# Kernel optimization log

Measured on AMD Instinct MI355X. Metric: run time of the kernel, lower is better.

Reference implementation:

```python
import jax, jax.numpy as jnp
import numpy as np

B, T, HD = 128, 256, 512
N_REAL, N_CAT, N_CLASSES, EMB = 32, 4, 100, 8
COMBINED = N_REAL + N_CAT * EMB  # 64
NEG_SLOPE = 0.1


def setup_inputs() -> dict:
    key = jax.random.key(0)
    ks = jax.random.split(key, 20)
    s = lambda *d: 1.0 / np.sqrt(d[0])
    real = jax.random.normal(ks[0], (B, T, N_REAL), dtype=jnp.float32)
    cats = jax.random.randint(ks[1], (B, T, N_CAT), 0, N_CLASSES).astype(jnp.float32)
    x0 = jnp.concatenate([real, cats], axis=-1)
    u = lambda k, shp, fan: jax.random.uniform(k, shp, jnp.float32, -1.0/np.sqrt(fan), 1.0/np.sqrt(fan))
    return {
        'x0': x0,
        'emb': jax.random.normal(ks[2], (N_CAT, N_CLASSES, EMB), dtype=jnp.float32),
        'W1': u(ks[3], (COMBINED, HD), COMBINED), 'b1': u(ks[4], (HD,), COMBINED),
        'W2': u(ks[5], (HD, HD), HD), 'b2': u(ks[6], (HD,), HD),
        'Wi_f': u(ks[7], (HD, 4 * HD), HD), 'bi_f': u(ks[8], (4 * HD,), HD),
        'Wh_f': u(ks[9], (HD, 4 * HD), HD), 'bh_f': u(ks[10], (4 * HD,), HD),
        'Wi_r': u(ks[11], (HD, 4 * HD), HD), 'bi_r': u(ks[12], (4 * HD,), HD),
        'Wh_r': u(ks[13], (HD, 4 * HD), HD), 'bh_r': u(ks[14], (4 * HD,), HD),
        'W3': u(ks[15], (2 * HD, 1), 2 * HD), 'b3': u(ks[16], (1,), 2 * HD),
    }


def leaky(x):
    return jnp.where(x >= 0, x, NEG_SLOPE * x)


def lstm(x, Wi, bi, Wh, bh):
    # x: [B, T, H] -> hidden states [B, T, H]
    b, t, h = x.shape
    xg = jnp.einsum('bti,ig->btg', x, Wi) + bi + bh  # precompute input contribution
    def step(carry, xg_t):
        hk, ck = carry
        g = xg_t + hk @ Wh  # [B, 4H]
        f, i, a, o = jnp.split(g, 4, axis=-1)
        ck = jax.nn.sigmoid(f) * ck + jax.nn.sigmoid(i) * jnp.tanh(a)
        hk = jax.nn.sigmoid(o) * jnp.tanh(ck)
        return (hk, ck), hk
    init = (jnp.zeros((b, h), x.dtype), jnp.zeros((b, h), x.dtype))
    _, hs = jax.lax.scan(step, init, jnp.swapaxes(xg, 0, 1))
    return jnp.swapaxes(hs, 0, 1)


def reference(x0, emb, W1, b1, W2, b2, Wi_f, bi_f, Wh_f, bh_f, Wi_r, bi_r, Wh_r, bh_r, W3, b3):
    real_part = x0[..., :N_REAL]
    idx = x0[..., N_REAL:N_REAL + N_CAT].astype(jnp.int32)  # [B, T, N_CAT]
    emb_out = emb[jnp.arange(N_CAT), idx]                    # [B, T, N_CAT, EMB]
    emb_out = emb_out.reshape(x0.shape[0], x0.shape[1], -1)
    combined = jnp.concatenate([real_part, emb_out], axis=-1)
    x1 = leaky(combined @ W1 + b1)
    x2 = leaky(x1 @ W2 + b2)
    h_f = lstm(x2, Wi_f, bi_f, Wh_f, bh_f)
    h_r = lstm(jnp.flip(x2, axis=1), Wi_r, bi_r, Wh_r, bh_r)
    x3 = jnp.concatenate([h_f, h_r], axis=-1)
    return x3 @ W3 + b3  # [B, T, 1]
```

## Files before the change

kernel.cpp:

```cpp
#include <hip/hip_runtime.h>
#include <cstddef>

namespace {

constexpr int B  = 128;
constexpr int T  = 256;
constexpr int HD = 512;
constexpr int G  = 2048;
constexpr int TC = 32;
constexpr int XIN = 36;
constexpr int NCHUNK = T / TC;

typedef __attribute__((ext_vector_type(8))) short short8;
typedef __attribute__((ext_vector_type(4))) short short4v;
typedef __attribute__((ext_vector_type(4))) float f32x4;

union U16B { uint4 u; short8 s; };

__device__ __forceinline__ float sigmf(float x) { return 1.0f / (1.0f + expf(-x)); }
__device__ __forceinline__ float leakyf(float x) { return x >= 0.0f ? x : 0.1f * x; }

__device__ __forceinline__ unsigned short f2bf(float v) {
  union { float f; unsigned u; } x; x.f = v;
  unsigned r = x.u + 0x7fffu + ((x.u >> 16) & 1u);
  return (unsigned short)(r >> 16);
}
__device__ __forceinline__ float bf2f(unsigned short b) {
  union { unsigned u; float f; } x; x.u = ((unsigned)b) << 16; return x.f;
}

__global__ void k_prep(const float* __restrict__ src, unsigned short* __restrict__ dh,
                       unsigned short* __restrict__ dl, int K, int N) {
  __shared__ float tile[32][33];
  const int n0 = blockIdx.x * 32, k0 = blockIdx.y * 32;
  for (int i = threadIdx.y; i < 32; i += 8)
    tile[i][threadIdx.x] = src[(size_t)(k0 + i) * N + n0 + threadIdx.x];
  __syncthreads();
  for (int i = threadIdx.y; i < 32; i += 8) {
    const float v = tile[threadIdx.x][i];
    const unsigned short h = f2bf(v);
    const size_t o = (size_t)(n0 + i) * K + k0 + threadIdx.x;
    dh[o] = h;
    dl[o] = f2bf(v - bf2f(h));
  }
}

__global__ void k_prep_pack(const float* __restrict__ Whf, const float* __restrict__ Whr,
                            unsigned short* __restrict__ wpkh, unsigned short* __restrict__ wpkl) {
  const int f = blockIdx.x * 256 + threadIdx.x;
  const int l  = f & 63;
  const int ks = (f >> 6) & 15;
  const int ct = (f >> 10) & 7;
  const int ut = (f >> 13) & 15;
  const int dir = f >> 17;
  const float* src = dir ? Whr : Whf;
  const int L = ct * 16 + (l & 15);
  const int gcol = (L >> 5) * HD + ut * 32 + (L & 31);
  const int k0 = ks * 32 + (l >> 4) * 8;
  short8 hv, lv;
  #pragma unroll
  for (int j = 0; j < 8; ++j) {
    const float v = src[(size_t)(k0 + j) * G + gcol];
    const unsigned short h = f2bf(v);
    hv[j] = (short)h;
    lv[j] = (short)f2bf(v - bf2f(h));
  }
  *(short8*)&wpkh[(size_t)f * 8] = hv;
  *(short8*)&wpkl[(size_t)f * 8] = lv;
}

__global__ void k_bias(const float* __restrict__ bif, const float* __restrict__ bhf,
                       const float* __restrict__ bir, const float* __restrict__ bhr,
                       float* __restrict__ biasI) {
  const int i = blockIdx.x * 256 + threadIdx.x;
  const int d = i >> 11, n = i & 2047;
  biasI[i] = (d ? bir[n] : bif[n]) + (d ? bhr[n] : bhf[n]);
}

__global__ void k_embed_gemm1(const float* __restrict__ x0, const float* __restrict__ emb,
                              const float* __restrict__ W1, const float* __restrict__ b1,
                              unsigned short* __restrict__ x1h, unsigned short* __restrict__ x1l) {
  __shared__ float As[64][65];
  __shared__ float Bs[64][68];
  const int tid = threadIdx.x;
  const int m0 = blockIdx.x * 64, n0 = blockIdx.y * 64;

  for (int i = tid; i < 64 * 64; i += 256) {
    const int m = i >> 6, k = i & 63;
    const size_t row = (size_t)(m0 + m);
    float v;
    if (k < 32) {
      v = x0[row * XIN + k];
    } else {
      const int c = (k - 32) >> 3, e = (k - 32) & 7;
      const int idx = (int)x0[row * XIN + 32 + c];
      v = emb[(size_t)(c * 100 + idx) * 8 + e];
    }
    As[m][k] = v;
  }
  for (int j = 0; j < 4; ++j) {
    const int q = tid + 256 * j;
    const int kk = q >> 4, nq = q & 15;
    *(float4*)&Bs[kk][nq * 4] = *(const float4*)&W1[(size_t)kk * HD + n0 + nq * 4];
  }
  __syncthreads();

  const int ty = tid >> 4, tx = tid & 15;
  float acc[4][4] = {};
  #pragma unroll 8
  for (int k = 0; k < 64; ++k) {
    const float a0 = As[ty * 4 + 0][k], a1 = As[ty * 4 + 1][k];
    const float a2 = As[ty * 4 + 2][k], a3 = As[ty * 4 + 3][k];
    const float4 bv = *(const float4*)&Bs[k][tx * 4];
    acc[0][0] += a0 * bv.x; acc[0][1] += a0 * bv.y; acc[0][2] += a0 * bv.z; acc[0][3] += a0 * bv.w;
    acc[1][0] += a1 * bv.x; acc[1][1] += a1 * bv.y; acc[1][2] += a1 * bv.z; acc[1][3] += a1 * bv.w;
    acc[2][0] += a2 * bv.x; acc[2][1] += a2 * bv.y; acc[2][2] += a2 * bv.z; acc[2][3] += a2 * bv.w;
    acc[3][0] += a3 * bv.x; acc[3][1] += a3 * bv.y; acc[3][2] += a3 * bv.z; acc[3][3] += a3 * bv.w;
  }
  const float4 b4 = *(const float4*)&b1[n0 + tx * 4];
  for (int i = 0; i < 4; ++i) {
    float o[4];
    o[0] = leakyf(acc[i][0] + b4.x);
    o[1] = leakyf(acc[i][1] + b4.y);
    o[2] = leakyf(acc[i][2] + b4.z);
    o[3] = leakyf(acc[i][3] + b4.w);
    short4v hv, lv;
    #pragma unroll
    for (int p = 0; p < 4; ++p) {
      const unsigned short hb = f2bf(o[p]);
      hv[p] = (short)hb;
      lv[p] = (short)f2bf(o[p] - bf2f(hb));
    }
    const size_t off = (size_t)(m0 + ty * 4 + i) * HD + n0 + tx * 4;
    *(short4v*)&x1h[off] = hv;
    *(short4v*)&x1l[off] = lv;
  }
}

template <int MODE>
__global__ __launch_bounds__(512) void k_mm(
    const unsigned short* __restrict__ Ah, const unsigned short* __restrict__ Al,
    const unsigned short* __restrict__ Bh, const unsigned short* __restrict__ Bl,
    const float* __restrict__ bias,
    unsigned short* __restrict__ oh, unsigned short* __restrict__ ol,
    float* __restrict__ of, int c0) {
  __shared__ unsigned short As_h[128 * 40], As_l[128 * 40];
  __shared__ unsigned short Bs_h[128 * 40], Bs_l[128 * 40];
  const int tid = threadIdx.x;
  const int m0 = blockIdx.x * 128, n0 = blockIdx.y * 128;
  const int dir = MODE ? (m0 >> 12) : 0;
  const unsigned short* Bhd = Bh + (size_t)dir * G * HD;
  const unsigned short* Bld = Bl + (size_t)dir * G * HD;

  const int si = tid >> 2, sseg = tid & 3;
  int arow;
  if (MODE) {
    const int r = m0 + si;
    const int tc = (r >> 7) & 31, bb = r & 127;
    const int tg = dir ? (T - 1 - (c0 + tc)) : (c0 + tc);
    arow = bb * T + tg;
  } else {
    arow = m0 + si;
  }
  const int brow = n0 + si;

  const int lane = tid & 63;
  const int c16 = lane & 15, q = lane >> 4;
  const int w = tid >> 6;
  const int mg = w & 3, ng = w >> 2;

  f32x4 acc[2][4] = {};

  for (int k0 = 0; k0 < HD; k0 += 32) {
    __syncthreads();
    *(short8*)&As_h[si * 40 + sseg * 8] = *(const short8*)&Ah[(size_t)arow * HD + k0 + sseg * 8];
    *(short8*)&As_l[si * 40 + sseg * 8] = *(const short8*)&Al[(size_t)arow * HD + k0 + sseg * 8];
    *(short8*)&Bs_h[si * 40 + sseg * 8] = *(const short8*)&Bhd[(size_t)brow * HD + k0 + sseg * 8];
    *(short8*)&Bs_l[si * 40 + sseg * 8] = *(const short8*)&Bld[(size_t)brow * HD + k0 + sseg * 8];
    __syncthreads();

    short8 ah[2], al[2], bh[4], bl[4];
    #pragma unroll
    for (int a = 0; a < 2; ++a) {
      const int rr = (2 * mg + a) * 16 + c16;
      ah[a] = *(const short8*)&As_h[rr * 40 + q * 8];
      al[a] = *(const short8*)&As_l[rr * 40 + q * 8];
    }
    #pragma unroll
    for (int j = 0; j < 4; ++j) {
      const int rr = (4 * ng + j) * 16 + c16;
      bh[j] = *(const short8*)&Bs_h[rr * 40 + q * 8];
      bl[j] = *(const short8*)&Bs_l[rr * 40 + q * 8];
    }
    #pragma unroll
    for (int a = 0; a < 2; ++a)
      #pragma unroll
      for (int j = 0; j < 4; ++j) {
        acc[a][j] = __builtin_amdgcn_mfma_f32_16x16x32_bf16(ah[a], bh[j], acc[a][j], 0, 0, 0);
        acc[a][j] = __builtin_amdgcn_mfma_f32_16x16x32_bf16(ah[a], bl[j], acc[a][j], 0, 0, 0);
        acc[a][j] = __builtin_amdgcn_mfma_f32_16x16x32_bf16(al[a], bh[j], acc[a][j], 0, 0, 0);
      }
  }

  #pragma unroll
  for (int a = 0; a < 2; ++a) {
    #pragma unroll
    for (int j = 0; j < 4; ++j) {
      const int nn = n0 + (4 * ng + j) * 16 + c16;
      const float bv = MODE ? bias[dir * G + nn] : bias[nn];
      #pragma unroll
      for (int r = 0; r < 4; ++r) {
        const int mm = m0 + (2 * mg + a) * 16 + 4 * q + r;
        float v = acc[a][j][r] + bv;
        if (MODE) {
          of[(size_t)mm * G + nn] = v;
        } else {
          v = leakyf(v);
          const unsigned short hb = f2bf(v);
          oh[(size_t)mm * HD + nn] = hb;
          ol[(size_t)mm * HD + nn] = f2bf(v - bf2f(hb));
        }
      }
    }
  }
}

__global__ __launch_bounds__(512, 2) void k_scan(
    const float* __restrict__ xg, const unsigned short* __restrict__ wpkh,
    const unsigned short* __restrict__ wpkl, unsigned int* __restrict__ hpk,
    float* __restrict__ cbuf, float* __restrict__ part,
    const float* __restrict__ W3, int* __restrict__ flags, int c0) {
  __shared__ unsigned int hst[16 * 516];
  __shared__ float gl[128 * 17];
  __shared__ float ysum[16 * 33];

  const int tid = threadIdx.x;
  const int bid = blockIdx.x;
  const int dir = bid >> 7;
  const int ut  = (bid >> 3) & 15;
  const int bt  = bid & 7;
  const int u0 = ut * 32, b0 = bt * 16;
  const int w = tid >> 6, lane = tid & 63;
  const int r16 = lane & 15, q = lane >> 4;

  const unsigned short* wp = wpkh + ((size_t)(((dir * 16 + ut) * 8 + w) * 16) << 9) + lane * 8;
  const unsigned short* wq = wpkl + ((size_t)(((dir * 16 + ut) * 8 + w) * 16) << 9) + lane * 8;
#define LDW(K) const short8 wh##K = *(const short8*)(wp + (K) * 512); \
               const short8 wl##K = *(const short8*)(wq + (K) * 512);
  LDW(0) LDW(1) LDW(2) LDW(3) LDW(4) LDW(5) LDW(6) LDW(7)
  LDW(8) LDW(9) LDW(10) LDW(11) LDW(12) LDW(13) LDW(14) LDW(15)
#undef LDW

  const int b_l = tid >> 5, u2 = tid & 31;
  const int bg = b0 + b_l, jg = u0 + u2;
  const size_t ci = ((size_t)dir * B + bg) * HD + jg;
  float creg = (c0 == 0) ? 0.0f : cbuf[ci];
  const float w3v = W3[dir * HD + jg];
  const int fl_base = dir * 8 + bt;
  const int hb = r16 * 516 + q * 8;

#define KSTEP(K) { \
    const uint4 aa = *(const uint4*)&hst[hb + (K) * 32]; \
    const uint4 bb = *(const uint4*)&hst[hb + (K) * 32 + 4]; \
    U16B hiu, lou; \
    hiu.u.x = __builtin_amdgcn_perm(aa.y, aa.x, 0x07060302u); \
    hiu.u.y = __builtin_amdgcn_perm(aa.w, aa.z, 0x07060302u); \
    hiu.u.z = __builtin_amdgcn_perm(bb.y, bb.x, 0x07060302u); \
    hiu.u.w = __builtin_amdgcn_perm(bb.w, bb.z, 0x07060302u); \
    lou.u.x = __builtin_amdgcn_perm(aa.y, aa.x, 0x05040100u); \
    lou.u.y = __builtin_amdgcn_perm(aa.w, aa.z, 0x05040100u); \
    lou.u.z = __builtin_amdgcn_perm(bb.y, bb.x, 0x05040100u); \
    lou.u.w = __builtin_amdgcn_perm(bb.w, bb.z, 0x05040100u); \
    acc = __builtin_amdgcn_mfma_f32_16x16x32_bf16(wh##K, hiu.s, acc, 0, 0, 0); \
    acc = __builtin_amdgcn_mfma_f32_16x16x32_bf16(wh##K, lou.s, acc, 0, 0, 0); \
    acc = __builtin_amdgcn_mfma_f32_16x16x32_bf16(wl##K, hiu.s, acc, 0, 0, 0); }

  for (int tc = 0; tc < TC; ++tc) {
    const int t = c0 + tc;

    const float* xr = xg + (((size_t)dir * TC + tc) * B + bg) * G;
    const float xgf = xr[jg];
    const float xgi = xr[HD + jg];
    const float xga = xr[2 * HD + jg];
    const float xgo = xr[3 * HD + jg];

    f32x4 acc = {0.0f, 0.0f, 0.0f, 0.0f};
    if (t > 0) {
      if (tc > 0) {
        if (tid == 0) {
          while (__hip_atomic_load(&flags[(t - 1) * 16 + fl_base], __ATOMIC_RELAXED,
                                   __HIP_MEMORY_SCOPE_AGENT) < 16)
            __builtin_amdgcn_s_sleep(1);
        }
        __syncthreads();
      }
      {
        const unsigned int* hsrc = hpk + ((size_t)((t & 1) * 2 + dir) * B + b0) * HD;
        unsigned int hv[16];
        #pragma unroll
        for (int i = 0; i < 16; ++i)
          hv[i] = __hip_atomic_load(&hsrc[i * HD + tid], __ATOMIC_RELAXED,
                                    __HIP_MEMORY_SCOPE_AGENT);
        #pragma unroll
        for (int i = 0; i < 16; ++i)
          hst[i * 516 + tid] = hv[i];
      }
      __syncthreads();
      KSTEP(0) KSTEP(1) KSTEP(2) KSTEP(3) KSTEP(4) KSTEP(5) KSTEP(6) KSTEP(7)
      KSTEP(8) KSTEP(9) KSTEP(10) KSTEP(11) KSTEP(12) KSTEP(13) KSTEP(14) KSTEP(15)
      __syncthreads();
    }

    gl[(w * 16 + q * 4 + 0) * 17 + r16] = acc[0];
    gl[(w * 16 + q * 4 + 1) * 17 + r16] = acc[1];
    gl[(w * 16 + q * 4 + 2) * 17 + r16] = acc[2];
    gl[(w * 16 + q * 4 + 3) * 17 + r16] = acc[3];
    __syncthreads();

    {
      const float gf = gl[(u2) * 17 + b_l]      + xgf;
      const float gi = gl[(32 + u2) * 17 + b_l] + xgi;
      const float ga = gl[(64 + u2) * 17 + b_l] + xga;
      const float go = gl[(96 + u2) * 17 + b_l] + xgo;
      const float cn = sigmf(gf) * creg + sigmf(gi) * tanhf(ga);
      const float hn = sigmf(go) * tanhf(cn);
      creg = cn;
      const unsigned short hh = f2bf(hn);
      const unsigned int hp = ((unsigned)hh << 16) | (unsigned)f2bf(hn - bf2f(hh));
      __hip_atomic_store(&hpk[((size_t)(((t + 1) & 1) * 2 + dir) * B + bg) * HD + jg], hp,
                         __ATOMIC_RELAXED, __HIP_MEMORY_SCOPE_AGENT);
      ysum[b_l * 33 + u2] = hn * w3v;
    }
    __syncthreads();

    if (tid == 0)
      __hip_atomic_fetch_add(&flags[t * 16 + fl_base], 1, __ATOMIC_RELAXED,
                             __HIP_MEMORY_SCOPE_AGENT);
    if (tid < 16) {
      float s = 0.0f;
      #pragma unroll
      for (int i = 0; i < 32; ++i) s += ysum[tid * 33 + i];
      part[((size_t)t * 32 + dir * 16 + ut) * B + b0 + tid] = s;
    }
  }
#undef KSTEP

  cbuf[ci] = creg;
}

__global__ void k_out(const float* __restrict__ part, const float* __restrict__ b3,
                      float* __restrict__ out) {
  const int o = blockIdx.x * 256 + threadIdx.x;
  const int b = o & 127, t = o >> 7;
  float s = b3[0];
  #pragma unroll
  for (int g = 0; g < 32; ++g) s += part[((size_t)t * 32 + g) * B + b];
  out[(size_t)b * T + t] = s;
}

}

extern "C" void kernel_launch(void* const* d_in, const int* in_sizes, int n_in,
                              void* d_out, int out_size, void* d_ws, size_t ws_size,
                              hipStream_t stream) {
  const float* x0   = (const float*)d_in[0];
  const float* emb  = (const float*)d_in[1];
  const float* W1   = (const float*)d_in[2];
  const float* b1   = (const float*)d_in[3];
  const float* W2   = (const float*)d_in[4];
  const float* b2   = (const float*)d_in[5];
  const float* Wi_f = (const float*)d_in[6];
  const float* bi_f = (const float*)d_in[7];
  const float* Wh_f = (const float*)d_in[8];
  const float* bh_f = (const float*)d_in[9];
  const float* Wi_r = (const float*)d_in[10];
  const float* bi_r = (const float*)d_in[11];
  const float* Wh_r = (const float*)d_in[12];
  const float* bh_r = (const float*)d_in[13];
  const float* W3   = (const float*)d_in[14];
  const float* b3   = (const float*)d_in[15];
  float* out = (float*)d_out;

  char* wsb = (char*)d_ws;
  unsigned short* x1h  = (unsigned short*)(wsb + 0);
  unsigned short* x1l  = (unsigned short*)(wsb + 33554432);
  float*          xgf  = (float*)(wsb + 0);
  unsigned short* x2h  = (unsigned short*)(wsb + 67108864);
  unsigned short* x2l  = (unsigned short*)(wsb + 100663296);
  unsigned short* wih  = (unsigned short*)(wsb + 134217728);
  unsigned short* wil  = (unsigned short*)(wsb + 138412032);
  unsigned short* w2h  = (unsigned short*)(wsb + 142606336);
  unsigned short* w2l  = (unsigned short*)(wsb + 143130624);
  unsigned short* wpkh = (unsigned short*)(wsb + 143654912);
  unsigned short* wpkl = (unsigned short*)(wsb + 147849216);
  unsigned int*   hpk  = (unsigned int*)(wsb + 152043520);
  float*          cbuf = (float*)(wsb + 153092096);
  float*          part = (float*)(wsb + 153616384);
  float*          bia  = (float*)(wsb + 157810688);
  int*            flg  = (int*)(wsb + 157827072);

  k_prep_pack<<<dim3(1024), 256, 0, stream>>>(Wh_f, Wh_r, wpkh, wpkl);
  k_prep<<<dim3(G / 32, HD / 32), dim3(32, 8), 0, stream>>>(Wi_f, wih, wil, HD, G);
  k_prep<<<dim3(G / 32, HD / 32), dim3(32, 8), 0, stream>>>(Wi_r, wih + (size_t)G * HD, wil + (size_t)G * HD, HD, G);
  k_prep<<<dim3(HD / 32, HD / 32), dim3(32, 8), 0, stream>>>(W2, w2h, w2l, HD, HD);
  k_bias<<<dim3(16), 256, 0, stream>>>(bi_f, bh_f, bi_r, bh_r, bia);

  hipMemsetAsync(flg, 0, T * 16 * sizeof(int), stream);

  k_embed_gemm1<<<dim3(B * T / 64, HD / 64), 256, 0, stream>>>(x0, emb, W1, b1, x1h, x1l);

  k_mm<0><<<dim3(B * T / 128, HD / 128), 512, 0, stream>>>(
      x1h, x1l, w2h, w2l, b2, x2h, x2l, nullptr, 0);

  void* args[9];
  int c0 = 0;
  args[0] = (void*)&xgf;  args[1] = (void*)&wpkh; args[2] = (void*)&wpkl;
  args[3] = (void*)&hpk;  args[4] = (void*)&cbuf; args[5] = (void*)&part;
  args[6] = (void*)&W3;   args[7] = (void*)&flg;  args[8] = (void*)&c0;

  for (int c = 0; c < NCHUNK; ++c) {
    c0 = c * TC;
    k_mm<1><<<dim3(2 * TC * B / 128, G / 128), 512, 0, stream>>>(
        x2h, x2l, wih, wil, bia, nullptr, nullptr, xgf, c0);
    hipLaunchCooperativeKernel((void*)k_scan, dim3(256), dim3(512), args, 0, stream);
  }

  k_out<<<dim3(B * T / 256), 256, 0, stream>>>(part, b3, out);
}
```

Measured before the change: 1.813 ms.

## Overlap next-chunk input-gate GEMM with LSTM scan using extra warps

The scan kernel grows to 1024 threads. The second half of each block computes the next chunk's input-gate GEMM tile into a double-buffered xg buffer while the first half runs the recurrent step, so the separate k_mm<1> launch per chunk is dropped. The chunk size is halved to fit the GEMM work into the per-timestep stages, and recurrent weights are now reloaded from memory on each K step instead of held in registers. Trade-offs are more syncthreads shared by both halves, more LDS use, and extra weight load traffic on the critical serial path.

```diff
diff --git a/kernel.cpp b/kernel.cpp
--- a/kernel.cpp
+++ b/kernel.cpp
@@ -7,7 +7,7 @@
 constexpr int T  = 256;
 constexpr int HD = 512;
 constexpr int G  = 2048;
-constexpr int TC = 32;
+constexpr int TC = 16;
 constexpr int XIN = 36;
 constexpr int NCHUNK = T / TC;
 
@@ -148,7 +148,7 @@
   __shared__ unsigned short Bs_h[128 * 40], Bs_l[128 * 40];
   const int tid = threadIdx.x;
   const int m0 = blockIdx.x * 128, n0 = blockIdx.y * 128;
-  const int dir = MODE ? (m0 >> 12) : 0;
+  const int dir = MODE ? (m0 / (TC * B)) : 0;
   const unsigned short* Bhd = Bh + (size_t)dir * G * HD;
   const unsigned short* Bld = Bl + (size_t)dir * G * HD;
 
@@ -156,7 +156,7 @@
   int arow;
   if (MODE) {
     const int r = m0 + si;
-    const int tc = (r >> 7) & 31, bb = r & 127;
+    const int tc = (r >> 7) & (TC - 1), bb = r & (B - 1);
     const int tg = dir ? (T - 1 - (c0 + tc)) : (c0 + tc);
     arow = bb * T + tg;
   } else {
@@ -225,41 +225,110 @@
   }
 }
 
-__global__ __launch_bounds__(512, 2) void k_scan(
-    const float* __restrict__ xg, const unsigned short* __restrict__ wpkh,
-    const unsigned short* __restrict__ wpkl, unsigned int* __restrict__ hpk,
-    float* __restrict__ cbuf, float* __restrict__ part,
-    const float* __restrict__ W3, int* __restrict__ flags, int c0) {
+__global__ __launch_bounds__(1024, 4) void k_scan2(
+    const float* __restrict__ xg, float* __restrict__ xgn,
+    const unsigned short* __restrict__ wpkh, const unsigned short* __restrict__ wpkl,
+    unsigned int* __restrict__ hpk, float* __restrict__ cbuf,
+    float* __restrict__ part, const float* __restrict__ W3,
+    int* __restrict__ flags, int c0,
+    const unsigned short* __restrict__ x2h, const unsigned short* __restrict__ x2l,
+    const unsigned short* __restrict__ wih, const unsigned short* __restrict__ wil,
+    const float* __restrict__ bia, int dog) {
   __shared__ unsigned int hst[16 * 516];
   __shared__ float gl[128 * 17];
   __shared__ float ysum[16 * 33];
-
-  const int tid = threadIdx.x;
-  const int bid = blockIdx.x;
+  __shared__ unsigned short gAh[128 * 40], gAl[128 * 40];
+  __shared__ unsigned short gBh[128 * 40], gBl[128 * 40];
+
+  const int tid  = threadIdx.x;
+  const int half = tid >> 9;
+  const int stid = tid & 511;
+  const int bid  = blockIdx.x;
+
   const int dir = bid >> 7;
   const int ut  = (bid >> 3) & 15;
   const int bt  = bid & 7;
   const int u0 = ut * 32, b0 = bt * 16;
-  const int w = tid >> 6, lane = tid & 63;
+  const int w = stid >> 6, lane = stid & 63;
   const int r16 = lane & 15, q = lane >> 4;
-
   const unsigned short* wp = wpkh + ((size_t)(((dir * 16 + ut) * 8 + w) * 16) << 9) + lane * 8;
   const unsigned short* wq = wpkl + ((size_t)(((dir * 16 + ut) * 8 + w) * 16) << 9) + lane * 8;
-#define LDW(K) const short8 wh##K = *(const short8*)(wp + (K) * 512); \
-               const short8 wl##K = *(const short8*)(wq + (K) * 512);
-  LDW(0) LDW(1) LDW(2) LDW(3) LDW(4) LDW(5) LDW(6) LDW(7)
-  LDW(8) LDW(9) LDW(10) LDW(11) LDW(12) LDW(13) LDW(14) LDW(15)
-#undef LDW
-
-  const int b_l = tid >> 5, u2 = tid & 31;
+
+  const int b_l = stid >> 5, u2 = stid & 31;
   const int bg = b0 + b_l, jg = u0 + u2;
   const size_t ci = ((size_t)dir * B + bg) * HD + jg;
-  float creg = (c0 == 0) ? 0.0f : cbuf[ci];
+  float creg = 0.0f;
+  if (half == 0 && c0 > 0) creg = cbuf[ci];
   const float w3v = W3[dir * HD + jg];
   const int fl_base = dir * 8 + bt;
   const int hb = r16 * 516 + q * 8;
 
+  const int gsi = stid >> 2, gseg = stid & 3;
+  const int gw = stid >> 6, glane = stid & 63;
+  const int gc16 = glane & 15, gq = glane >> 4;
+  const int gmg = gw & 3, gng = gw >> 2;
+  const int c0n = c0 + TC;
+  f32x4 gacc[2][4] = {};
+
+#define GEMM_STAGE(g) { \
+    const int tt = bid * 2 + ((g) >> 4); const int ls = (g) & 15; \
+    const int m0g = (tt & 31) * 128, n0g = (tt >> 5) * 128; \
+    const int dirg = m0g >> 11; \
+    const int rr0 = m0g + gsi; \
+    const int tcc = (rr0 >> 7) & (TC - 1), bb2 = rr0 & (B - 1); \
+    const int tg = dirg ? (T - 1 - (c0n + tcc)) : (c0n + tcc); \
+    const int arow = bb2 * T + tg; \
+    const int brow = n0g + gsi; \
+    const int k0g = ls * 32; \
+    const unsigned short* Bh2 = wih + (size_t)dirg * G * HD; \
+    const unsigned short* Bl2 = wil + (size_t)dirg * G * HD; \
+    *(short8*)&gAh[gsi * 40 + gseg * 8] = *(const short8*)&x2h[(size_t)arow * HD + k0g + gseg * 8]; \
+    *(short8*)&gAl[gsi * 40 + gseg * 8] = *(const short8*)&x2l[(size_t)arow * HD + k0g + gseg * 8]; \
+    *(short8*)&gBh[gsi * 40 + gseg * 8] = *(const short8*)&Bh2[(size_t)brow * HD + k0g + gseg * 8]; \
+    *(short8*)&gBl[gsi * 40 + gseg * 8] = *(const short8*)&Bl2[(size_t)brow * HD + k0g + gseg * 8]; }
+
+#define GEMM_MFMA(g) { \
+    const int ls = (g) & 15; \
+    if (ls == 0) { \
+      _Pragma("unroll") for (int a = 0; a < 2; ++a) \
+        _Pragma("unroll") for (int j = 0; j < 4; ++j) \
+          gacc[a][j] = (f32x4){0.f, 0.f, 0.f, 0.f}; \
+    } \
+    short8 ah[2], al[2], bh4[4], bl4[4]; \
+    _Pragma("unroll") for (int a = 0; a < 2; ++a) { \
+      const int rr = (2 * gmg + a) * 16 + gc16; \
+      ah[a] = *(const short8*)&gAh[rr * 40 + gq * 8]; \
+      al[a] = *(const short8*)&gAl[rr * 40 + gq * 8]; \
+    } \
+    _Pragma("unroll") for (int j = 0; j < 4; ++j) { \
+      const int rr = (4 * gng + j) * 16 + gc16; \
+      bh4[j] = *(const short8*)&gBh[rr * 40 + gq * 8]; \
+      bl4[j] = *(const short8*)&gBl[rr * 40 + gq * 8]; \
+    } \
+    _Pragma("unroll") for (int a = 0; a < 2; ++a) \
+      _Pragma("unroll") for (int j = 0; j < 4; ++j) { \
+        gacc[a][j] = __builtin_amdgcn_mfma_f32_16x16x32_bf16(ah[a], bh4[j], gacc[a][j], 0, 0, 0); \
+        gacc[a][j] = __builtin_amdgcn_mfma_f32_16x16x32_bf16(ah[a], bl4[j], gacc[a][j], 0, 0, 0); \
+        gacc[a][j] = __builtin_amdgcn_mfma_f32_16x16x32_bf16(al[a], bh4[j], gacc[a][j], 0, 0, 0); \
+      } \
+    if (ls == 15) { \
+      const int tt = bid * 2 + ((g) >> 4); \
+      const int m0g = (tt & 31) * 128, n0g = (tt >> 5) * 128; \
+      const int dirg = m0g >> 11; \
+      _Pragma("unroll") for (int a = 0; a < 2; ++a) \
+        _Pragma("unroll") for (int j = 0; j < 4; ++j) { \
+          const int nn = n0g + (4 * gng + j) * 16 + gc16; \
+          const float bv = bia[dirg * G + nn]; \
+          _Pragma("unroll") for (int r = 0; r < 4; ++r) { \
+            const int mm = m0g + (2 * gmg + a) * 16 + 4 * gq + r; \
+            xgn[(size_t)mm * G + nn] = gacc[a][j][r] + bv; \
+          } \
+        } \
+    } }
+
 #define KSTEP(K) { \
+    const short8 whv = *(const short8*)(wp + (K) * 512); \
+    const short8 wlv = *(const short8*)(wq + (K) * 512); \
     const uint4 aa = *(const uint4*)&hst[hb + (K) * 32]; \
     const uint4 bb = *(const uint4*)&hst[hb + (K) * 32 + 4]; \
     U16B hiu, lou; \
@@ -271,53 +340,69 @@
     lou.u.y = __builtin_amdgcn_perm(aa.w, aa.z, 0x05040100u); \
     lou.u.z = __builtin_amdgcn_perm(bb.y, bb.x, 0x05040100u); \
     lou.u.w = __builtin_amdgcn_perm(bb.w, bb.z, 0x05040100u); \
-    acc = __builtin_amdgcn_mfma_f32_16x16x32_bf16(wh##K, hiu.s, acc, 0, 0, 0); \
-    acc = __builtin_amdgcn_mfma_f32_16x16x32_bf16(wh##K, lou.s, acc, 0, 0, 0); \
-    acc = __builtin_amdgcn_mfma_f32_16x16x32_bf16(wl##K, hiu.s, acc, 0, 0, 0); }
+    acc = __builtin_amdgcn_mfma_f32_16x16x32_bf16(whv, hiu.s, acc, 0, 0, 0); \
+    acc = __builtin_amdgcn_mfma_f32_16x16x32_bf16(whv, lou.s, acc, 0, 0, 0); \
+    acc = __builtin_amdgcn_mfma_f32_16x16x32_bf16(wlv, hiu.s, acc, 0, 0, 0); }
 
   for (int tc = 0; tc < TC; ++tc) {
     const int t = c0 + tc;
-
-    const float* xr = xg + (((size_t)dir * TC + tc) * B + bg) * G;
-    const float xgf = xr[jg];
-    const float xgi = xr[HD + jg];
-    const float xga = xr[2 * HD + jg];
-    const float xgo = xr[3 * HD + jg];
-
+    float xgf = 0.f, xgi = 0.f, xga = 0.f, xgo = 0.f;
     f32x4 acc = {0.0f, 0.0f, 0.0f, 0.0f};
-    if (t > 0) {
-      if (tc > 0) {
-        if (tid == 0) {
-          while (__hip_atomic_load(&flags[(t - 1) * 16 + fl_base], __ATOMIC_RELAXED,
-                                   __HIP_MEMORY_SCOPE_AGENT) < 16)
-            __builtin_amdgcn_s_sleep(1);
-        }
-        __syncthreads();
+
+    if (half == 0) {
+      const float* xr = xg + (((size_t)dir * TC + tc) * B + bg) * G;
+      xgf = xr[jg];
+      xgi = xr[HD + jg];
+      xga = xr[2 * HD + jg];
+      xgo = xr[3 * HD + jg];
+      if (tc > 0 && stid == 0) {
+        while (__hip_atomic_load(&flags[(t - 1) * 16 + fl_base], __ATOMIC_RELAXED,
+                                 __HIP_MEMORY_SCOPE_AGENT) < 16)
+          __builtin_amdgcn_s_sleep(1);
       }
-      {
+    } else if (dog) {
+      GEMM_STAGE(2 * tc)
+    }
+    __syncthreads();
+
+    if (half == 0) {
+      if (t > 0) {
         const unsigned int* hsrc = hpk + ((size_t)((t & 1) * 2 + dir) * B + b0) * HD;
         unsigned int hv[16];
         #pragma unroll
         for (int i = 0; i < 16; ++i)
-          hv[i] = __hip_atomic_load(&hsrc[i * HD + tid], __ATOMIC_RELAXED,
+          hv[i] = __hip_atomic_load(&hsrc[i * HD + stid], __ATOMIC_RELAXED,
                                     __HIP_MEMORY_SCOPE_AGENT);
         #pragma unroll
         for (int i = 0; i < 16; ++i)
-          hst[i * 516 + tid] = hv[i];
+          hst[i * 516 + stid] = hv[i];
       }
-      __syncthreads();
-      KSTEP(0) KSTEP(1) KSTEP(2) KSTEP(3) KSTEP(4) KSTEP(5) KSTEP(6) KSTEP(7)
-      KSTEP(8) KSTEP(9) KSTEP(10) KSTEP(11) KSTEP(12) KSTEP(13) KSTEP(14) KSTEP(15)
-      __syncthreads();
-    }
-
-    gl[(w * 16 + q * 4 + 0) * 17 + r16] = acc[0];
-    gl[(w * 16 + q * 4 + 1) * 17 + r16] = acc[1];
-    gl[(w * 16 + q * 4 + 2) * 17 + r16] = acc[2];
-    gl[(w * 16 + q * 4 + 3) * 17 + r16] = acc[3];
-    __syncthreads();
-
-    {
+    } else if (dog) {
+      GEMM_MFMA(2 * tc)
+    }
+    __syncthreads();
+
+    if (half == 0) {
+      if (t > 0) {
+        KSTEP(0) KSTEP(1) KSTEP(2) KSTEP(3) KSTEP(4) KSTEP(5) KSTEP(6) KSTEP(7)
+        KSTEP(8) KSTEP(9) KSTEP(10) KSTEP(11) KSTEP(12) KSTEP(13) KSTEP(14) KSTEP(15)
+      }
+    } else if (dog) {
+      GEMM_STAGE(2 * tc + 1)
+    }
+    __syncthreads();
+
+    if (half == 0) {
+      gl[(w * 16 + q * 4 + 0) * 17 + r16] = acc[0];
+      gl[(w * 16 + q * 4 + 1) * 17 + r16] = acc[1];
+      gl[(w * 16 + q * 4 + 2) * 17 + r16] = acc[2];
+      gl[(w * 16 + q * 4 + 3) * 17 + r16] = acc[3];
+    } else if (dog) {
+      GEMM_MFMA(2 * tc + 1)
+    }
+    __syncthreads();
+
+    if (half == 0) {
       const float gf = gl[(u2) * 17 + b_l]      + xgf;
       const float gi = gl[(32 + u2) * 17 + b_l] + xgi;
       const float ga = gl[(64 + u2) * 17 + b_l] + xga;
@@ -333,19 +418,23 @@
     }
     __syncthreads();
 
-    if (tid == 0)
-      __hip_atomic_fetch_add(&flags[t * 16 + fl_base], 1, __ATOMIC_RELAXED,
-                             __HIP_MEMORY_SCOPE_AGENT);
-    if (tid < 16) {
-      float s = 0.0f;
-      #pragma unroll
-      for (int i = 0; i < 32; ++i) s += ysum[tid * 33 + i];
-      part[((size_t)t * 32 + dir * 16 + ut) * B + b0 + tid] = s;
+    if (half == 0) {
+      if (stid == 0)
+        __hip_atomic_fetch_add(&flags[t * 16 + fl_base], 1, __ATOMIC_RELAXED,
+                               __HIP_MEMORY_SCOPE_AGENT);
+      if (stid < 16) {
+        float s = 0.0f;
+        #pragma unroll
+        for (int i = 0; i < 32; ++i) s += ysum[stid * 33 + i];
+        part[((size_t)t * 32 + dir * 16 + ut) * B + b0 + stid] = s;
+      }
     }
   }
 #undef KSTEP
-
-  cbuf[ci] = creg;
+#undef GEMM_MFMA
+#undef GEMM_STAGE
+
+  if (half == 0) cbuf[ci] = creg;
 }
 
 __global__ void k_out(const float* __restrict__ part, const float* __restrict__ b3,
@@ -384,7 +473,8 @@
   char* wsb = (char*)d_ws;
   unsigned short* x1h  = (unsigned short*)(wsb + 0);
   unsigned short* x1l  = (unsigned short*)(wsb + 33554432);
-  float*          xgf  = (float*)(wsb + 0);
+  float*          xgA  = (float*)(wsb + 0);
+  float*          xgB  = (float*)(wsb + 33554432);
   unsigned short* x2h  = (unsigned short*)(wsb + 67108864);
   unsigned short* x2l  = (unsigned short*)(wsb + 100663296);
   unsigned short* wih  = (unsigned short*)(wsb + 134217728);
@@ -412,17 +502,29 @@
   k_mm<0><<<dim3(B * T / 128, HD / 128), 512, 0, stream>>>(
       x1h, x1l, w2h, w2l, b2, x2h, x2l, nullptr, 0);
 
-  void* args[9];
-  int c0 = 0;
-  args[0] = (void*)&xgf;  args[1] = (void*)&wpkh; args[2] = (void*)&wpkl;
-  args[3] = (void*)&hpk;  args[4] = (void*)&cbuf; args[5] = (void*)&part;
-  args[6] = (void*)&W3;   args[7] = (void*)&flg;  args[8] = (void*)&c0;
+  k_mm<1><<<dim3(2 * TC * B / 128, G / 128), 512, 0, stream>>>(
+      x2h, x2l, wih, wil, bia, nullptr, nullptr, xgA, 0);
+
+  float* xgbuf[2] = {xgA, xgB};
+  const float* xg_cur;
+  float* xg_nxt;
+  int c0 = 0, dog = 1;
+  void* args[16];
+  args[0]  = (void*)&xg_cur; args[1]  = (void*)&xg_nxt;
+  args[2]  = (void*)&wpkh;   args[3]  = (void*)&wpkl;
+  args[4]  = (void*)&hpk;    args[5]  = (void*)&cbuf;
+  args[6]  = (void*)&part;   args[7]  = (void*)&W3;
+  args[8]  = (void*)&flg;    args[9]  = (void*)&c0;
+  args[10] = (void*)&x2h;    args[11] = (void*)&x2l;
+  args[12] = (void*)&wih;    args[13] = (void*)&wil;
+  args[14] = (void*)&bia;    args[15] = (void*)&dog;
 
   for (int c = 0; c < NCHUNK; ++c) {
     c0 = c * TC;
-    k_mm<1><<<dim3(2 * TC * B / 128, G / 128), 512, 0, stream>>>(
-        x2h, x2l, wih, wil, bia, nullptr, nullptr, xgf, c0);
-    hipLaunchCooperativeKernel((void*)k_scan, dim3(256), dim3(512), args, 0, stream);
+    dog = (c + 1 < NCHUNK) ? 1 : 0;
+    xg_cur = xgbuf[c & 1];
+    xg_nxt = xgbuf[(c + 1) & 1];
+    hipLaunchCooperativeKernel((void*)k_scan2, dim3(256), dim3(1024), args, 0, stream);
   }
 
   k_out<<<dim3(B * T / 256), 256, 0, stream>>>(part, b3, out);
```

After: 5.410 ms. 2.98x slower.
